# Performance work log

Measured on AMD Instinct MI355X. Metric: run time of the kernel, lower is better.

The kernel has to match this reference:

```python
import jax, jax.numpy as jnp
import numpy as np

H = 8          # heads
EPS = 1e-5     # BatchNorm eps
NEG_SLOPE = 0.2


def setup_inputs() -> dict:
    key = jax.random.key(0)
    ks = jax.random.split(key, 7)
    B, Cin, N, Cout, k = 4, 128, 8192, 256, 32
    x = jax.random.normal(ks[0], (B, Cin, N), dtype=jnp.float32)
    edges = jax.random.randint(ks[1], (B, N, k), 0, N, dtype=jnp.int64)
    Wq = jax.random.normal(ks[2], (Cout, Cin), dtype=jnp.float32) * 0.05
    Wk = jax.random.normal(ks[3], (Cout, Cin), dtype=jnp.float32) * 0.05
    Wv = jax.random.normal(ks[4], (Cout, Cin), dtype=jnp.float32) * 0.05
    Wo = jax.random.normal(ks[5], (Cout, Cout), dtype=jnp.float32) * 0.05
    gamma = jnp.ones((Cout,), dtype=jnp.float32)
    beta = jnp.zeros((Cout,), dtype=jnp.float32)
    return {"x": x, "edges": edges, "Wq": Wq, "Wk": Wk, "Wv": Wv,
            "Wo": Wo, "gamma": gamma, "beta": beta}


def reference(x, edges, Wq, Wk, Wv, Wo, gamma, beta):
    B, C, N = x.shape
    Cout = Wq.shape[0]
    hd = Cout // H
    # 1x1 convs == channel matmuls
    Q = jnp.einsum('oc,bcn->bon', Wq, x)   # [B,Cout,N]
    K = jnp.einsum('oc,bcn->bon', Wk, x)
    V = jnp.einsum('oc,bcn->bon', Wv, x)
    # split heads: Cout -> (H, hd)
    Qh = Q.reshape(B, H, hd, N).transpose(0, 1, 3, 2)   # [B,H,N,hd]
    Kt = K.reshape(B, H, hd, N).transpose(0, 3, 1, 2)   # [B,N,H,hd]
    Vt = V.reshape(B, H, hd, N).transpose(0, 3, 1, 2)   # [B,N,H,hd]
    # gather k neighbors per node (per batch element)
    gather = jax.vmap(lambda pts, idx: pts[idx])        # [B,N,k,H,hd]
    Kn = gather(Kt, edges)
    Vn = gather(Vt, edges)
    # local attention over the k neighbors
    scores = jnp.einsum('bhnd,bnkhd->bhnk', Qh, Kn) / jnp.sqrt(
        jnp.asarray(hd, dtype=x.dtype))
    w = jax.nn.softmax(scores, axis=-1)                 # [B,H,N,k]
    att = jnp.einsum('bhnk,bnkhd->bhnd', w, Vn)         # [B,H,N,hd]
    feat = att.transpose(0, 1, 3, 2).reshape(B, Cout, N)
    # out conv -> BatchNorm1d (training-mode batch stats) -> LeakyReLU
    o = jnp.einsum('oc,bcn->bon', Wo, feat)
    mean = jnp.mean(o, axis=(0, 2), keepdims=True)
    var = jnp.var(o, axis=(0, 2), keepdims=True)        # biased, as torch BN
    o = (o - mean) / jnp.sqrt(var + EPS)
    o = gamma[None, :, None] * o + beta[None, :, None]
    return jnp.where(o >= 0, o, NEG_SLOPE * o)
```

## Files before the change

### kernel.cpp

```cpp
#include <hip/hip_runtime.h>
#include <math.h>

#define HEADS 8
#define KNB 32
#define CIN 128
#define COUT 256
#define BB 4
#define NN 8192
#define EPSV 1e-5f
#define SLOPE 0.2f

typedef _Float16 h8 __attribute__((ext_vector_type(8)));
typedef _Float16 h4 __attribute__((ext_vector_type(4)));
typedef float f4 __attribute__((ext_vector_type(4)));

__global__ __launch_bounds__(256) void qkv_kernel(
    const float* __restrict__ x,
    const float* __restrict__ Wq, const float* __restrict__ Wk, const float* __restrict__ Wv,
    _Float16* __restrict__ Q, _Float16* __restrict__ K, _Float16* __restrict__ V)
{
    __shared__ _Float16 wl[16][65][8];
    __shared__ _Float16 xl[16][65][8];
    const int t = threadIdx.x;
    const int i = blockIdx.x;
    const int xcd = i & 7;
    const int local = i >> 3;
    const int matco = local % 12;
    const int tl = local / 12;
    const int g = tl * 8 + xcd;
    const int b = g >> 7;
    const int n0 = (g & 127) << 6;
    const int mat = matco >> 2;
    const int co0 = (matco & 3) << 6;
    const float* __restrict__ W = (mat == 0) ? Wq : (mat == 1) ? Wk : Wv;

#pragma unroll
    for (int it = 0; it < 8; ++it) {
        const int flat = t + it * 256;
        const int co = flat >> 5;
        const int k4 = (flat & 31) << 2;
        float4 wv = *(const float4*)(W + (size_t)(co0 + co) * CIN + k4);
        h4 hv; hv[0] = (_Float16)wv.x; hv[1] = (_Float16)wv.y;
        hv[2] = (_Float16)wv.z; hv[3] = (_Float16)wv.w;
        *(h4*)&wl[k4 >> 3][co][k4 & 7] = hv;
    }
#pragma unroll
    for (int it = 0; it < 8; ++it) {
        const int flat = t + it * 256;
        const int ci = flat >> 4;
        const int n4 = (flat & 15) << 2;
        float4 xv = *(const float4*)(x + ((size_t)b * CIN + ci) * NN + n0 + n4);
        xl[ci >> 3][n4 + 0][ci & 7] = (_Float16)xv.x;
        xl[ci >> 3][n4 + 1][ci & 7] = (_Float16)xv.y;
        xl[ci >> 3][n4 + 2][ci & 7] = (_Float16)xv.z;
        xl[ci >> 3][n4 + 3][ci & 7] = (_Float16)xv.w;
    }
    __syncthreads();

    const int w = t >> 6, lane = t & 63;
    const int m = lane & 15, ko = lane >> 4;
    f4 acc[4];
#pragma unroll
    for (int j = 0; j < 4; ++j) acc[j] = (f4){0.f, 0.f, 0.f, 0.f};
#pragma unroll
    for (int s = 0; s < 4; ++s) {
        const h8 a = *(const h8*)&wl[s * 4 + ko][w * 16 + m][0];
#pragma unroll
        for (int j = 0; j < 4; ++j) {
            const h8 bb = *(const h8*)&xl[s * 4 + ko][j * 16 + m][0];
            acc[j] = __builtin_amdgcn_mfma_f32_16x16x32_f16(a, bb, acc[j], 0, 0, 0);
        }
    }

    _Float16* __restrict__ Y = (mat == 0) ? Q : (mat == 1) ? K : V;
    const int cob = co0 + w * 16 + (lane >> 4) * 4;
#pragma unroll
    for (int j = 0; j < 4; ++j) {
        const int n = n0 + j * 16 + m;
        h4 hv; hv[0] = (_Float16)acc[j][0]; hv[1] = (_Float16)acc[j][1];
        hv[2] = (_Float16)acc[j][2]; hv[3] = (_Float16)acc[j][3];
        *(h4*)(Y + ((size_t)b * NN + n) * COUT + cob) = hv;
    }
}

__global__ __launch_bounds__(256) void attn_kernel(
    const _Float16* __restrict__ Q, const _Float16* __restrict__ K, const _Float16* __restrict__ V,
    const int* __restrict__ edges, _Float16* __restrict__ feat)
{
    __shared__ float s_sc[4][HEADS][33];
    __shared__ float s_w[4][HEADS][33];
    __shared__ int s_idx[4][KNB];
    const int t = threadIdx.x;
    const int wv = t >> 6;
    const int lane = t & 63;
    const int b = blockIdx.y;
    const int n = (blockIdx.x << 2) + wv;
    const int h = lane >> 3;
    const int dg = lane & 7;
    const size_t nb = (size_t)b * NN;
    const size_t base = (nb + n) * COUT;
    const int c = lane * 4;

    const h4 qh = __builtin_nontemporal_load((const h4*)(Q + base + c));
    const float scl = 0.17677669529663688f;
    const float qx = (float)qh[0] * scl, qy = (float)qh[1] * scl;
    const float qz = (float)qh[2] * scl, qw = (float)qh[3] * scl;
    if (lane < KNB) s_idx[wv][lane] = __builtin_nontemporal_load(edges + (nb + n) * KNB + lane);
    __syncthreads();

    const _Float16* __restrict__ Kp = K + nb * COUT;
    const _Float16* __restrict__ Vp = V + nb * COUT;

#pragma unroll
    for (int j = 0; j < KNB; ++j) {
        const h4 kh = *(const h4*)(Kp + (size_t)s_idx[wv][j] * COUT + c);
        float p = qx * (float)kh[0] + qy * (float)kh[1] + qz * (float)kh[2] + qw * (float)kh[3];
        p += __shfl_xor(p, 1, 8);
        p += __shfl_xor(p, 2, 8);
        p += __shfl_xor(p, 4, 8);
        if (dg == 0) s_sc[wv][h][j] = p;
    }
    __syncthreads();

#pragma unroll
    for (int g = 0; g < 4; ++g) {
        const int id = g * 64 + lane;
        const int hh = id >> 5, jj = id & 31;
        float val = s_sc[wv][hh][jj];
        float mx = val;
        mx = fmaxf(mx, __shfl_xor(mx, 16, 32));
        mx = fmaxf(mx, __shfl_xor(mx, 8, 32));
        mx = fmaxf(mx, __shfl_xor(mx, 4, 32));
        mx = fmaxf(mx, __shfl_xor(mx, 2, 32));
        mx = fmaxf(mx, __shfl_xor(mx, 1, 32));
        float e = __expf(val - mx);
        float s = e;
        s += __shfl_xor(s, 16, 32);
        s += __shfl_xor(s, 8, 32);
        s += __shfl_xor(s, 4, 32);
        s += __shfl_xor(s, 2, 32);
        s += __shfl_xor(s, 1, 32);
        s_w[wv][hh][jj] = e / s;
    }
    __syncthreads();

    float ax = 0.f, ay = 0.f, az = 0.f, aw = 0.f;
#pragma unroll
    for (int j = 0; j < KNB; ++j) {
        const float w = s_w[wv][h][j];
        const h4 vh = *(const h4*)(Vp + (size_t)s_idx[wv][j] * COUT + c);
        ax += w * (float)vh[0]; ay += w * (float)vh[1];
        az += w * (float)vh[2]; aw += w * (float)vh[3];
    }
    h4 f; f[0] = (_Float16)ax; f[1] = (_Float16)ay; f[2] = (_Float16)az; f[3] = (_Float16)aw;
    __builtin_nontemporal_store(f, (h4*)(feat + base + c));
}

__global__ __launch_bounds__(256) void wo_kernel(
    const _Float16* __restrict__ feat, const float* __restrict__ Wo, float* __restrict__ o)
{
    __shared__ _Float16 wl[16][65][8];
    __shared__ _Float16 fl[16][65][8];
    const int t = threadIdx.x;
    const int i = blockIdx.x;
    const int xcd = i & 7;
    const int local = i >> 3;
    const int co0 = (local & 3) << 6;
    const int tl = local >> 2;
    const int g = tl * 8 + xcd;
    const int b = g >> 7;
    const int n0 = (g & 127) << 6;
    const int w = t >> 6, lane = t & 63;
    const int m = lane & 15, ko = lane >> 4;
    f4 acc[4];
#pragma unroll
    for (int j = 0; j < 4; ++j) acc[j] = (f4){0.f, 0.f, 0.f, 0.f};

    for (int c0 = 0; c0 < COUT; c0 += 128) {
#pragma unroll
        for (int it = 0; it < 8; ++it) {
            const int flat = t + it * 256;
            const int co = flat >> 5;
            const int k4 = (flat & 31) << 2;
            float4 wv = *(const float4*)(Wo + (size_t)(co0 + co) * COUT + c0 + k4);
            h4 hv; hv[0] = (_Float16)wv.x; hv[1] = (_Float16)wv.y;
            hv[2] = (_Float16)wv.z; hv[3] = (_Float16)wv.w;
            *(h4*)&wl[k4 >> 3][co][k4 & 7] = hv;
        }
#pragma unroll
        for (int it = 0; it < 4; ++it) {
            const int flat = t + it * 256;
            const int n = flat >> 4;
            const int c8 = flat & 15;
            const h8 fv = *(const h8*)(feat + ((size_t)b * NN + n0 + n) * COUT + c0 + c8 * 8);
            *(h8*)&fl[c8][n][0] = fv;
        }
        __syncthreads();
#pragma unroll
        for (int s = 0; s < 4; ++s) {
            const h8 a = *(const h8*)&wl[s * 4 + ko][w * 16 + m][0];
#pragma unroll
            for (int j = 0; j < 4; ++j) {
                const h8 bb = *(const h8*)&fl[s * 4 + ko][j * 16 + m][0];
                acc[j] = __builtin_amdgcn_mfma_f32_16x16x32_f16(a, bb, acc[j], 0, 0, 0);
            }
        }
        __syncthreads();
    }

    const int cob = co0 + w * 16 + (lane >> 4) * 4;
#pragma unroll
    for (int j = 0; j < 4; ++j) {
        const int n = n0 + j * 16 + m;
        *(f4*)(o + ((size_t)b * NN + n) * COUT + cob) = acc[j];
    }
}

__global__ __launch_bounds__(256) void bn_part(const float* __restrict__ o,
                                               float* __restrict__ ps, float* __restrict__ pss)
{
    const int blk = blockIdx.x;
    const int co = threadIdx.x;
    float s = 0.f, ss = 0.f;
    const size_t r0 = (size_t)blk * 64;
    for (int r = 0; r < 64; ++r) {
        const float v = o[(r0 + r) * COUT + co];
        s += v; ss += v * v;
    }
    ps[blk * COUT + co] = s;
    pss[blk * COUT + co] = ss;
}

__global__ __launch_bounds__(256) void bn_reduce(const float* __restrict__ ps, const float* __restrict__ pss,
                                                 const float* __restrict__ gamma, const float* __restrict__ beta,
                                                 float* __restrict__ stats)
{
    const int co = threadIdx.x;
    float s = 0.f, ss = 0.f;
    for (int p = 0; p < 512; ++p) { s += ps[p * COUT + co]; ss += pss[p * COUT + co]; }
    const float inv = 1.f / (float)(BB * NN);
    const float mean = s * inv;
    const float var = ss * inv - mean * mean;
    const float istd = rsqrtf(var + EPSV);
    const float sc = gamma[co] * istd;
    stats[co * 2] = sc;
    stats[co * 2 + 1] = beta[co] - mean * sc;
}

__global__ __launch_bounds__(256) void bn_apply(const float* __restrict__ o,
                                                const float* __restrict__ stats,
                                                float* __restrict__ out)
{
    __shared__ float tile[64][68];
    const int i = blockIdx.x;
    const int nt_ = i & 127, ct = (i >> 7) & 3, b = i >> 9;
    const int n0 = nt_ << 6, co0 = ct << 6;
    const int t = threadIdx.x;
    const int cq = (t & 15) << 2, rg = t >> 4;
#pragma unroll
    for (int it = 0; it < 4; ++it) {
        const int n = rg + it * 16;
        f4 v = *(const f4*)(o + ((size_t)b * NN + n0 + n) * COUT + co0 + cq);
        *(f4*)&tile[n][cq] = v;
    }
    __syncthreads();
    const int n4 = (t & 15) << 2, cg = t >> 4;
#pragma unroll
    for (int it = 0; it < 4; ++it) {
        const int co = cg + it * 16;
        const float sc = stats[(co0 + co) * 2];
        const float sh = stats[(co0 + co) * 2 + 1];
        f4 r;
#pragma unroll
        for (int j = 0; j < 4; ++j) {
            float v = sc * tile[n4 + j][co] + sh;
            r[j] = (v >= 0.f) ? v : SLOPE * v;
        }
        *(f4*)(out + ((size_t)b * COUT + co0 + co) * NN + n0 + n4) = r;
    }
}

extern "C" void kernel_launch(void* const* d_in, const int* in_sizes, int n_in,
                              void* d_out, int out_size, void* d_ws, size_t ws_size,
                              hipStream_t stream)
{
    const float* x     = (const float*)d_in[0];
    const int*   edges = (const int*)d_in[1];
    const float* Wq    = (const float*)d_in[2];
    const float* Wk    = (const float*)d_in[3];
    const float* Wv    = (const float*)d_in[4];
    const float* Wo    = (const float*)d_in[5];
    const float* gamma = (const float*)d_in[6];
    const float* beta  = (const float*)d_in[7];
    float* out = (float*)d_out;

    const size_t SZ = (size_t)BB * NN * COUT;
    _Float16* Q    = (_Float16*)d_ws;
    _Float16* K    = Q + SZ;
    _Float16* V    = K + SZ;
    float*    o    = (float*)(V + SZ);
    float*    ps   = o + SZ;
    float*    pss  = ps + 512 * COUT;
    float*    stats = pss + 512 * COUT;
    _Float16* feat = Q;

    qkv_kernel<<<dim3(12 * 128 * BB), 256, 0, stream>>>(x, Wq, Wk, Wv, Q, K, V);
    attn_kernel<<<dim3(NN / 4, BB), 256, 0, stream>>>(Q, K, V, edges, feat);
    wo_kernel<<<dim3(4 * 128 * BB), 256, 0, stream>>>(feat, Wo, o);
    bn_part<<<dim3(512), 256, 0, stream>>>(o, ps, pss);
    bn_reduce<<<dim3(1), 256, 0, stream>>>(ps, pss, gamma, beta, stats);
    bn_apply<<<dim3(2048), 256, 0, stream>>>(o, stats, out);
}
```

Measured before the change: 283.7 us.

## Fuse BN statistics into Wo epilogue and split attention into score/PV kernels

The separate bn_part and bn_reduce passes are removed. Per-channel sum and sum-of-squares are now reduced inside the wo_kernel epilogue with shuffles and global atomics. The accumulators are zeroed by block 0 of qkv_kernel, and the scale and shift are computed per block in bn_apply. This avoids re-reading the full fp32 output and drops two launches. The attention kernel is split in two: one kernel writes fp16 softmax weights to a new workspace buffer, and a second gathers V using those weights. This isolates the K and V gather passes, at the cost of an extra write and read of the weight buffer and one more launch. The x load in qkv_kernel is also rewritten to read four channels at once and store packed h4 values to LDS.

Measured after the change: 288.8 us. No clear change (+1.8%).

```diff
diff --git a/kernel.cpp b/kernel.cpp
--- a/kernel.cpp
+++ b/kernel.cpp
@@ -17,11 +17,13 @@
 __global__ __launch_bounds__(256) void qkv_kernel(
     const float* __restrict__ x,
     const float* __restrict__ Wq, const float* __restrict__ Wk, const float* __restrict__ Wv,
-    _Float16* __restrict__ Q, _Float16* __restrict__ K, _Float16* __restrict__ V)
+    _Float16* __restrict__ Q, _Float16* __restrict__ K, _Float16* __restrict__ V,
+    float* __restrict__ pz)
 {
     __shared__ _Float16 wl[16][65][8];
     __shared__ _Float16 xl[16][65][8];
     const int t = threadIdx.x;
+    if (blockIdx.x == 0) { pz[t] = 0.f; pz[t + 256] = 0.f; }
     const int i = blockIdx.x;
     const int xcd = i & 7;
     const int local = i >> 3;
@@ -45,15 +47,20 @@
         *(h4*)&wl[k4 >> 3][co][k4 & 7] = hv;
     }
 #pragma unroll
-    for (int it = 0; it < 8; ++it) {
+    for (int it = 0; it < 2; ++it) {
         const int flat = t + it * 256;
-        const int ci = flat >> 4;
+        const int ci = (flat >> 4) << 2;
         const int n4 = (flat & 15) << 2;
-        float4 xv = *(const float4*)(x + ((size_t)b * CIN + ci) * NN + n0 + n4);
-        xl[ci >> 3][n4 + 0][ci & 7] = (_Float16)xv.x;
-        xl[ci >> 3][n4 + 1][ci & 7] = (_Float16)xv.y;
-        xl[ci >> 3][n4 + 2][ci & 7] = (_Float16)xv.z;
-        xl[ci >> 3][n4 + 3][ci & 7] = (_Float16)xv.w;
+        const f4 x0 = *(const f4*)(x + ((size_t)b * CIN + ci + 0) * NN + n0 + n4);
+        const f4 x1 = *(const f4*)(x + ((size_t)b * CIN + ci + 1) * NN + n0 + n4);
+        const f4 x2 = *(const f4*)(x + ((size_t)b * CIN + ci + 2) * NN + n0 + n4);
+        const f4 x3 = *(const f4*)(x + ((size_t)b * CIN + ci + 3) * NN + n0 + n4);
+#pragma unroll
+        for (int j = 0; j < 4; ++j) {
+            h4 hv; hv[0] = (_Float16)x0[j]; hv[1] = (_Float16)x1[j];
+            hv[2] = (_Float16)x2[j]; hv[3] = (_Float16)x3[j];
+            *(h4*)&xl[ci >> 3][n4 + j][ci & 7] = hv;
+        }
     }
     __syncthreads();
 
@@ -73,7 +80,7 @@
     }
 
     _Float16* __restrict__ Y = (mat == 0) ? Q : (mat == 1) ? K : V;
-    const int cob = co0 + w * 16 + (lane >> 4) * 4;
+    const int cob = co0 + w * 16 + ko * 4;
 #pragma unroll
     for (int j = 0; j < 4; ++j) {
         const int n = n0 + j * 16 + m;
@@ -83,12 +90,11 @@
     }
 }
 
-__global__ __launch_bounds__(256) void attn_kernel(
-    const _Float16* __restrict__ Q, const _Float16* __restrict__ K, const _Float16* __restrict__ V,
-    const int* __restrict__ edges, _Float16* __restrict__ feat)
+__global__ __launch_bounds__(256) void attn_scores(
+    const _Float16* __restrict__ Q, const _Float16* __restrict__ K,
+    const int* __restrict__ edges, _Float16* __restrict__ wbuf)
 {
     __shared__ float s_sc[4][HEADS][33];
-    __shared__ float s_w[4][HEADS][33];
     __shared__ int s_idx[4][KNB];
     const int t = threadIdx.x;
     const int wv = t >> 6;
@@ -109,8 +115,6 @@
     __syncthreads();
 
     const _Float16* __restrict__ Kp = K + nb * COUT;
-    const _Float16* __restrict__ Vp = V + nb * COUT;
-
 #pragma unroll
     for (int j = 0; j < KNB; ++j) {
         const h4 kh = *(const h4*)(Kp + (size_t)s_idx[wv][j] * COUT + c);
@@ -140,10 +144,39 @@
         s += __shfl_xor(s, 4, 32);
         s += __shfl_xor(s, 2, 32);
         s += __shfl_xor(s, 1, 32);
-        s_w[wv][hh][jj] = e / s;
-    }
-    __syncthreads();
-
+        __builtin_nontemporal_store((_Float16)(e / s), wbuf + base + id);
+    }
+}
+
+__global__ __launch_bounds__(256) void attn_pv(
+    const _Float16* __restrict__ V, const _Float16* __restrict__ wbuf,
+    const int* __restrict__ edges, _Float16* __restrict__ feat)
+{
+    __shared__ float s_w[4][HEADS][33];
+    __shared__ int s_idx[4][KNB];
+    const int t = threadIdx.x;
+    const int wv = t >> 6;
+    const int lane = t & 63;
+    const int b = blockIdx.y;
+    const int n = (blockIdx.x << 2) + wv;
+    const int h = lane >> 3;
+    const size_t nb = (size_t)b * NN;
+    const size_t base = (nb + n) * COUT;
+    const int c = lane * 4;
+
+    if (lane < KNB) s_idx[wv][lane] = __builtin_nontemporal_load(edges + (nb + n) * KNB + lane);
+    {
+        const h4 wh = __builtin_nontemporal_load((const h4*)(wbuf + base + c));
+        const int hh = lane >> 3;
+        const int jj = (lane * 4) & 31;
+        s_w[wv][hh][jj + 0] = (float)wh[0];
+        s_w[wv][hh][jj + 1] = (float)wh[1];
+        s_w[wv][hh][jj + 2] = (float)wh[2];
+        s_w[wv][hh][jj + 3] = (float)wh[3];
+    }
+    __syncthreads();
+
+    const _Float16* __restrict__ Vp = V + nb * COUT;
     float ax = 0.f, ay = 0.f, az = 0.f, aw = 0.f;
 #pragma unroll
     for (int j = 0; j < KNB; ++j) {
@@ -157,7 +190,8 @@
 }
 
 __global__ __launch_bounds__(256) void wo_kernel(
-    const _Float16* __restrict__ feat, const float* __restrict__ Wo, float* __restrict__ o)
+    const _Float16* __restrict__ feat, const float* __restrict__ Wo, float* __restrict__ o,
+    float* __restrict__ ps, float* __restrict__ pss)
 {
     __shared__ _Float16 wl[16][65][8];
     __shared__ _Float16 fl[16][65][8];
@@ -208,54 +242,56 @@
         __syncthreads();
     }
 
-    const int cob = co0 + w * 16 + (lane >> 4) * 4;
+    const int cob = co0 + w * 16 + ko * 4;
 #pragma unroll
     for (int j = 0; j < 4; ++j) {
         const int n = n0 + j * 16 + m;
         *(f4*)(o + ((size_t)b * NN + n) * COUT + cob) = acc[j];
     }
-}
-
-__global__ __launch_bounds__(256) void bn_part(const float* __restrict__ o,
-                                               float* __restrict__ ps, float* __restrict__ pss)
-{
-    const int blk = blockIdx.x;
-    const int co = threadIdx.x;
-    float s = 0.f, ss = 0.f;
-    const size_t r0 = (size_t)blk * 64;
-    for (int r = 0; r < 64; ++r) {
-        const float v = o[(r0 + r) * COUT + co];
-        s += v; ss += v * v;
-    }
-    ps[blk * COUT + co] = s;
-    pss[blk * COUT + co] = ss;
-}
-
-__global__ __launch_bounds__(256) void bn_reduce(const float* __restrict__ ps, const float* __restrict__ pss,
-                                                 const float* __restrict__ gamma, const float* __restrict__ beta,
-                                                 float* __restrict__ stats)
-{
-    const int co = threadIdx.x;
-    float s = 0.f, ss = 0.f;
-    for (int p = 0; p < 512; ++p) { s += ps[p * COUT + co]; ss += pss[p * COUT + co]; }
-    const float inv = 1.f / (float)(BB * NN);
-    const float mean = s * inv;
-    const float var = ss * inv - mean * mean;
-    const float istd = rsqrtf(var + EPSV);
-    const float sc = gamma[co] * istd;
-    stats[co * 2] = sc;
-    stats[co * 2 + 1] = beta[co] - mean * sc;
+
+    float s_[4], ss_[4];
+#pragma unroll
+    for (int r = 0; r < 4; ++r) {
+        float sv = acc[0][r] + acc[1][r] + acc[2][r] + acc[3][r];
+        float qv = acc[0][r] * acc[0][r] + acc[1][r] * acc[1][r]
+                 + acc[2][r] * acc[2][r] + acc[3][r] * acc[3][r];
+#pragma unroll
+        for (int d = 1; d < 16; d <<= 1) {
+            sv += __shfl_xor(sv, d, 16);
+            qv += __shfl_xor(qv, d, 16);
+        }
+        s_[r] = sv; ss_[r] = qv;
+    }
+    if (m == 0) {
+#pragma unroll
+        for (int r = 0; r < 4; ++r) {
+            atomicAdd(&ps[cob + r], s_[r]);
+            atomicAdd(&pss[cob + r], ss_[r]);
+        }
+    }
 }
 
 __global__ __launch_bounds__(256) void bn_apply(const float* __restrict__ o,
-                                                const float* __restrict__ stats,
-                                                float* __restrict__ out)
+    const float* __restrict__ ps, const float* __restrict__ pss,
+    const float* __restrict__ gamma, const float* __restrict__ beta,
+    float* __restrict__ out)
 {
     __shared__ float tile[64][68];
+    __shared__ float s_sc[64], s_sh[64];
     const int i = blockIdx.x;
     const int nt_ = i & 127, ct = (i >> 7) & 3, b = i >> 9;
     const int n0 = nt_ << 6, co0 = ct << 6;
     const int t = threadIdx.x;
+    if (t < 64) {
+        const int co = co0 + t;
+        const float inv = 1.f / (float)(BB * NN);
+        const float mean = ps[co] * inv;
+        const float var = pss[co] * inv - mean * mean;
+        const float istd = rsqrtf(var + EPSV);
+        const float sc = gamma[co] * istd;
+        s_sc[t] = sc;
+        s_sh[t] = beta[co] - mean * sc;
+    }
     const int cq = (t & 15) << 2, rg = t >> 4;
 #pragma unroll
     for (int it = 0; it < 4; ++it) {
@@ -268,8 +304,8 @@
 #pragma unroll
     for (int it = 0; it < 4; ++it) {
         const int co = cg + it * 16;
-        const float sc = stats[(co0 + co) * 2];
-        const float sh = stats[(co0 + co) * 2 + 1];
+        const float sc = s_sc[co];
+        const float sh = s_sh[co];
         f4 r;
 #pragma unroll
         for (int j = 0; j < 4; ++j) {
@@ -298,16 +334,15 @@
     _Float16* Q    = (_Float16*)d_ws;
     _Float16* K    = Q + SZ;
     _Float16* V    = K + SZ;
-    float*    o    = (float*)(V + SZ);
+    _Float16* wbuf = V + SZ;
+    float*    o    = (float*)(wbuf + SZ);
     float*    ps   = o + SZ;
-    float*    pss  = ps + 512 * COUT;
-    float*    stats = pss + 512 * COUT;
+    float*    pss  = ps + COUT;
     _Float16* feat = Q;
 
-    qkv_kernel<<<dim3(12 * 128 * BB), 256, 0, stream>>>(x, Wq, Wk, Wv, Q, K, V);
-    attn_kernel<<<dim3(NN / 4, BB), 256, 0, stream>>>(Q, K, V, edges, feat);
-    wo_kernel<<<dim3(4 * 128 * BB), 256, 0, stream>>>(feat, Wo, o);
-    bn_part<<<dim3(512), 256, 0, stream>>>(o, ps, pss);
-    bn_reduce<<<dim3(1), 256, 0, stream>>>(ps, pss, gamma, beta, stats);
-    bn_apply<<<dim3(2048), 256, 0, stream>>>(o, stats, out);
-}
+    qkv_kernel<<<dim3(12 * 128 * BB), 256, 0, stream>>>(x, Wq, Wk, Wv, Q, K, V, ps);
+    attn_scores<<<dim3(NN / 4, BB), 256, 0, stream>>>(Q, K, edges, wbuf);
+    attn_pv<<<dim3(NN / 4, BB), 256, 0, stream>>>(V, wbuf, edges, feat);
+    wo_kernel<<<dim3(4 * 128 * BB), 256, 0, stream>>>(feat, Wo, o, ps, pss);
+    bn_apply<<<dim3(2048), 256, 0, stream>>>(o, ps, pss, gamma, beta, out);
+}
```
